# Kernel tuning notes

Measured on AMD Instinct MI355X. Metric: run time of the kernel, lower is better.

Reference implementation:

```python
import jax, jax.numpy as jnp
import numpy as np

B, L, V = 16, 2048, 64


def setup_inputs() -> dict:
    key = jax.random.key(0)
    k1, k2, k3, k4 = jax.random.split(key, 4)
    idx = jax.random.randint(k1, (B, L), 0, V)                      # tokens
    Wq_w = jax.random.normal(k2, (V, V), jnp.float32) * 0.02         # nn.Linear weight
    Wv_w = jax.random.normal(k3, (V, V), jnp.float32) * 0.02 + np.float32(np.e)  # Wv.weight (+e init)
    v_emb = jax.random.normal(k4, (L, 1), jnp.float32) * 0.02        # nn.Embedding(length, 1)
    return {"idx": idx, "Wq_w": Wq_w, "Wv_w": Wv_w, "v_emb": v_emb}


def reference(idx, Wq_w, Wv_w, v_emb):
    Lx = v_emb.shape[0]
    Vx = Wq_w.shape[0]
    # e = one_hot token embedding, [B, L, V]
    e = jax.nn.one_hot(idx, Vx, dtype=jnp.float32)
    i = jnp.arange(Lx)
    # pos[i, j] = max(i - j, 0); learned relative-position score table [L, L]
    pos = jnp.maximum(i[:, None] - i[None, :], 0)
    pos_embd = v_emb[pos, 0]
    causal = i[:, None] >= i[None, :]                                # tril mask
    # Attention block 1: scores are the learned position table (no QK^T)
    attn1 = jax.nn.softmax(jnp.where(causal, pos_embd, -jnp.inf), axis=-1)  # [L, L]
    l1 = jnp.einsum('ts,bsv->btv', attn1, e)                         # [B, L, V]
    # Attention block 2: Wq(e) @ l1^T, masked softmax, attn @ e * scalar
    q = jnp.einsum('btv,uv->btu', e, Wq_w)                           # F.linear: e @ Wq^T
    scores = jnp.einsum('btv,bsv->bts', q, l1)                       # [B, L, L]
    attn2 = jax.nn.softmax(jnp.where(causal, scores, -jnp.inf), axis=-1)
    l2 = jnp.einsum('bts,bsv->btv', attn2, e) * Wv_w[0, 0]           # logits [B, L, V]
    return l2
```

## Files before the change

### kernel.cpp

```cpp
#include <hip/hip_runtime.h>


#define LSEQ 2048
#define NB 16
#define NV 64
#define NC 32

typedef __attribute__((ext_vector_type(8))) short bf16x8;
typedef __attribute__((ext_vector_type(4))) float f32x4;

__device__ __forceinline__ unsigned short f2bf(float f) {
  unsigned int u = __float_as_uint(f);
  return (unsigned short)((u + 0x7FFFu + ((u >> 16) & 1u)) >> 16);
}

__global__ __launch_bounds__(256) void k_gather(const int* __restrict__ idx,
                                                const float* __restrict__ Wq,
                                                const float* __restrict__ v_emb,
                                                unsigned short* __restrict__ Agr,
                                                unsigned short* __restrict__ Ebf,
                                                float* __restrict__ S) {
  const int b = blockIdx.x >> 4;
  const int tile = blockIdx.x & 15;
  const int w = threadIdx.x >> 6;
  const int lane = threadIdx.x & 63;

  if (blockIdx.x == 0 && threadIdx.x < 64) {
    const int base = lane * 32;
    float e[32];
    float run = 0.f;
#pragma unroll
    for (int i = 0; i < 32; ++i) { e[i] = expf(v_emb[base + i]); run += e[i]; }
    float incl = run;
#pragma unroll
    for (int d = 1; d < 64; d <<= 1) {
      float up = __shfl_up(incl, d);
      if (lane >= d) incl += up;
    }
    float acc = incl - run;
#pragma unroll
    for (int i = 0; i < 32; ++i) {
      acc += e[i];
      Ebf[base + i] = f2bf(e[i]);
      S[base + i] = acc;
    }
  }

  const int k8base = tile * 16 + w * 4;
#pragma unroll
  for (int r = 0; r < 4; ++r) {
    const int k8 = k8base + r;
    unsigned short v[8];
#pragma unroll
    for (int j = 0; j < 8; ++j) {
      const int ii = idx[b * LSEQ + (2047 - (k8 * 8 + j))];
      v[j] = f2bf(Wq[ii * 64 + lane]);
    }
    uint4 st;
    st.x = (unsigned int)v[0] | ((unsigned int)v[1] << 16);
    st.y = (unsigned int)v[2] | ((unsigned int)v[3] << 16);
    st.z = (unsigned int)v[4] | ((unsigned int)v[5] << 16);
    st.w = (unsigned int)v[6] | ((unsigned int)v[7] << 16);
    *(uint4*)(Agr + ((size_t)(b * 256 + k8) * 64 + lane) * 8) = st;
  }
}

__global__ __launch_bounds__(256) void k_gemm(const unsigned short* __restrict__ Agr,
                                              const unsigned short* __restrict__ Ebf,
                                              const float* __restrict__ S,
                                              float* __restrict__ P) {
  __shared__ unsigned short GL0[2208];
  __shared__ unsigned short GL1[2176];
  __shared__ float red[16][64];
  __shared__ float red2[16][64];

  const int b  = blockIdx.y;
  const int bn = 63 - (int)blockIdx.x;
  const int n0 = bn * 32;
  const int tid = threadIdx.x;
  const int w = tid >> 6;
  const int lane = tid & 63;
  const int quad = lane >> 4;
  const int lm = lane & 15;
  const int nsub = w & 1;
  const int kh = w >> 1;

  {
    const int wend = n0 + 160;
    for (int i = 96 + tid; i < wend; i += 256) {
      const int e0 = i - 127;
      const int e1 = i - 126;
      GL0[i] = (e0 >= 0 && e0 < LSEQ) ? Ebf[e0] : (unsigned short)0;
      GL1[i] = (e1 >= 0 && e1 < LSEQ) ? Ebf[e1] : (unsigned short)0;
    }
  }
  __syncthreads();

  f32x4 acc[4];
#pragma unroll
  for (int mt = 0; mt < 4; ++mt) acc[mt] = (f32x4){0.f, 0.f, 0.f, 0.f};

  const int nbase = n0 + nsub * 16;
  const int sbase = nbase + lm - 1920;
  const int kstart = 2048 - (n0 + 32);
  const int iters = bn + 1;
  const unsigned short* __restrict__ abase = Agr + (size_t)b * 256 * 64 * 8;

  union AF { uint4 u; bf16x8 v; };
  union BF { unsigned int u[4]; bf16x8 v; };
  AF a[3][4];
  BF bb[3];

#define LOAD_FRAGS(J_, SL) do {                                             \
    const int k_ = kstart + (kh + 2 * (J_)) * 32;                           \
    const int kq8_ = (k_ >> 3) + quad;                                      \
    const unsigned short* ab_ = abase + ((size_t)kq8_ * 64 + lm) * 8;       \
    a[SL][0].u = *(const uint4*)(ab_ + 0 * 128);                            \
    a[SL][1].u = *(const uint4*)(ab_ + 1 * 128);                            \
    a[SL][2].u = *(const uint4*)(ab_ + 2 * 128);                            \
    a[SL][3].u = *(const uint4*)(ab_ + 3 * 128);                            \
    const int s_ = sbase + k_ + quad * 8;                                   \
    const unsigned int* gb_ = (s_ & 1) ? (const unsigned int*)GL1           \
                                       : (const unsigned int*)GL0;          \
    const int off_ = s_ >> 1;                                               \
    bb[SL].u[0] = gb_[off_ + 0]; bb[SL].u[1] = gb_[off_ + 1];               \
    bb[SL].u[2] = gb_[off_ + 2]; bb[SL].u[3] = gb_[off_ + 3];               \
  } while (0)

#define MFMA4(SL) do {                                                      \
    acc[0] = __builtin_amdgcn_mfma_f32_16x16x32_bf16(a[SL][0].v, bb[SL].v, acc[0], 0, 0, 0); \
    acc[1] = __builtin_amdgcn_mfma_f32_16x16x32_bf16(a[SL][1].v, bb[SL].v, acc[1], 0, 0, 0); \
    acc[2] = __builtin_amdgcn_mfma_f32_16x16x32_bf16(a[SL][2].v, bb[SL].v, acc[2], 0, 0, 0); \
    acc[3] = __builtin_amdgcn_mfma_f32_16x16x32_bf16(a[SL][3].v, bb[SL].v, acc[3], 0, 0, 0); \
  } while (0)

  const int J = (iters > kh) ? ((iters - kh + 1) >> 1) : 0;
  if (J > 0) {
    LOAD_FRAGS(0, 0);
    if (J > 1) LOAD_FRAGS(1, 1);
    int j = 0;
    while (true) {
      if (j + 2 < J) LOAD_FRAGS(j + 2, 2);
      MFMA4(0);
      if (++j >= J) break;
      if (j + 2 < J) LOAD_FRAGS(j + 2, 0);
      MFMA4(1);
      if (++j >= J) break;
      if (j + 2 < J) LOAD_FRAGS(j + 2, 1);
      MFMA4(2);
      if (++j >= J) break;
    }
  }
#undef LOAD_FRAGS
#undef MFMA4

  if (kh == 1) {
    float (*rd)[64] = nsub ? red2 : red;
#pragma unroll
    for (int mt = 0; mt < 4; ++mt)
#pragma unroll
      for (int r = 0; r < 4; ++r) rd[mt * 4 + r][lane] = acc[mt][r];
  }
  __syncthreads();
  if (kh == 0) {
    float (*rd)[64] = nsub ? red2 : red;
#pragma unroll
    for (int mt = 0; mt < 4; ++mt)
#pragma unroll
      for (int r = 0; r < 4; ++r) acc[mt][r] += rd[mt * 4 + r][lane];

    const float sinv = 1.0f / S[nbase + lm];
#pragma unroll
    for (int mt = 0; mt < 4; ++mt) {
#pragma unroll
      for (int r = 0; r < 4; ++r) {
        const int c = mt * 16 + quad * 4 + r;
        P[((size_t)(b * 64 + c)) * LSEQ + nbase + lm] = __expf(acc[mt][r] * sinv);
      }
    }
  }
}

__global__ __launch_bounds__(256) void k_scanemit(const int* __restrict__ idx,
                                                  const float* __restrict__ P,
                                                  const float* __restrict__ Wv,
                                                  float* __restrict__ out) {
  __shared__ float Hs[NC][65];
  __shared__ float bins[4][64];
  const int bc = blockIdx.x;
  const int b = bc >> 6;
  const int c = bc & 63;
  const int w = threadIdx.x >> 6;
  const int lane = threadIdx.x & 63;

  const float* __restrict__ prow = P + (size_t)bc * LSEQ;
  const int* __restrict__ irow = idx + b * LSEQ;

  float p[8]; int ii[8];
#pragma unroll
  for (int r = 0; r < 8; ++r) {
    const int ch = w * 8 + r;
    p[r] = prow[ch * 64 + lane];
    ii[r] = irow[ch * 64 + lane];
  }
  for (int i = threadIdx.x; i < NC * 65; i += 256) ((float*)Hs)[i] = 0.f;
  __syncthreads();
#pragma unroll
  for (int r = 0; r < 8; ++r) atomicAdd(&Hs[w * 8 + r][ii[r]], p[r]);
  __syncthreads();

  const int half = lane >> 5, l32 = lane & 31;
#pragma unroll
  for (int r = 0; r < 8; ++r) {
    const int v = w * 16 + r * 2 + half;
    const float h = Hs[l32][v];
    float x = h;
#pragma unroll
    for (int d = 1; d < 32; d <<= 1) {
      float up = __shfl_up(x, d, 32);
      if (l32 >= d) x += up;
    }
    Hs[l32][v] = x - h;
  }
  __syncthreads();

  const float wv = Wv[0];
#pragma unroll
  for (int r = 0; r < 8; ++r) {
    const int ch = w * 8 + r;
    unsigned long long m = __ballot(ii[r] == c);
    while (m) {
      const int srel = __builtin_ctzll(m);
      m &= m - 1;
      const int t = ch * 64 + srel;
      const float pm = (lane <= srel) ? p[r] : 0.f;
      bins[w][lane] = 0.f;
      __threadfence_block();
      atomicAdd(&bins[w][ii[r]], pm);
      __threadfence_block();
      const float bin = bins[w][lane] + Hs[ch][lane];
      float z = bin;
#pragma unroll
      for (int d = 1; d < 64; d <<= 1) z += __shfl_xor(z, d);
      out[((size_t)(b * LSEQ + t)) * 64 + lane] = wv * bin / z;
    }
  }
}

extern "C" void kernel_launch(void* const* d_in, const int* in_sizes, int n_in,
                              void* d_out, int out_size, void* d_ws, size_t ws_size,
                              hipStream_t stream) {
  const int* idx     = (const int*)d_in[0];
  const float* Wq    = (const float*)d_in[1];
  const float* Wv    = (const float*)d_in[2];
  const float* v_emb = (const float*)d_in[3];
  float* out = (float*)d_out;

  float* S = (float*)d_ws;
  float* P = S + LSEQ;
  unsigned short* Ebf = (unsigned short*)(P + (size_t)NB * NV * LSEQ);
  unsigned short* Agr = Ebf + LSEQ;

  k_gather<<<NB * 16, 256, 0, stream>>>(idx, Wq, v_emb, Agr, Ebf, S);
  k_gemm<<<dim3(64, NB), 256, 0, stream>>>(Agr, Ebf, S, P);
  k_scanemit<<<NB * NV, 256, 0, stream>>>(idx, P, Wv, out);
}
```

Measured before the change: 120.3 us.

## Halve GEMM N-tile and split M across waves to double block count

The GEMM kernel now uses 16-column N tiles instead of 32, launching 128x16 blocks. Each wave pair splits the 64 output channels in half (msub) rather than splitting N. Pipelining drops from triple to double buffering, and launch bounds request 8 blocks per CU. The aim is better load balance across CUs for the triangular causal workload and lower register pressure. The cost is more redundant A-fragment loads and a shallower prefetch.

```diff
diff --git a/kernel.cpp b/kernel.cpp
--- a/kernel.cpp
+++ b/kernel.cpp
@@ -65,28 +65,27 @@
   }
 }
 
-__global__ __launch_bounds__(256) void k_gemm(const unsigned short* __restrict__ Agr,
-                                              const unsigned short* __restrict__ Ebf,
-                                              const float* __restrict__ S,
-                                              float* __restrict__ P) {
+__global__ __launch_bounds__(256, 8) void k_gemm(const unsigned short* __restrict__ Agr,
+                                                 const unsigned short* __restrict__ Ebf,
+                                                 const float* __restrict__ S,
+                                                 float* __restrict__ P) {
   __shared__ unsigned short GL0[2208];
   __shared__ unsigned short GL1[2176];
-  __shared__ float red[16][64];
-  __shared__ float red2[16][64];
+  __shared__ float red[2][8][64];
 
   const int b  = blockIdx.y;
-  const int bn = 63 - (int)blockIdx.x;
-  const int n0 = bn * 32;
+  const int bn = 127 - (int)blockIdx.x;
+  const int n0 = bn * 16;
   const int tid = threadIdx.x;
   const int w = tid >> 6;
   const int lane = tid & 63;
   const int quad = lane >> 4;
   const int lm = lane & 15;
-  const int nsub = w & 1;
+  const int msub = w & 1;
   const int kh = w >> 1;
 
   {
-    const int wend = n0 + 160;
+    const int wend = n0 + 144;
     for (int i = 96 + tid; i < wend; i += 256) {
       const int e0 = i - 127;
       const int e1 = i - 126;
@@ -96,86 +95,72 @@
   }
   __syncthreads();
 
-  f32x4 acc[4];
-#pragma unroll
-  for (int mt = 0; mt < 4; ++mt) acc[mt] = (f32x4){0.f, 0.f, 0.f, 0.f};
-
-  const int nbase = n0 + nsub * 16;
-  const int sbase = nbase + lm - 1920;
-  const int kstart = 2048 - (n0 + 32);
-  const int iters = bn + 1;
+  f32x4 acc[2];
+  acc[0] = (f32x4){0.f, 0.f, 0.f, 0.f};
+  acc[1] = (f32x4){0.f, 0.f, 0.f, 0.f};
+
+  const int sbase = n0 + lm - 1920;
+  const int kext = (n0 + 16 + 31) & ~31;
+  const int kstart = 2048 - kext;
+  const int iters = kext >> 5;
   const unsigned short* __restrict__ abase = Agr + (size_t)b * 256 * 64 * 8;
+  const unsigned int* __restrict__ gb =
+      (sbase & 1) ? (const unsigned int*)GL1 : (const unsigned int*)GL0;
 
   union AF { uint4 u; bf16x8 v; };
   union BF { unsigned int u[4]; bf16x8 v; };
-  AF a[3][4];
-  BF bb[3];
+  AF a[2][2];
+  BF bb[2];
 
 #define LOAD_FRAGS(J_, SL) do {                                             \
     const int k_ = kstart + (kh + 2 * (J_)) * 32;                           \
     const int kq8_ = (k_ >> 3) + quad;                                      \
-    const unsigned short* ab_ = abase + ((size_t)kq8_ * 64 + lm) * 8;       \
+    const unsigned short* ab_ = abase + ((size_t)kq8_ * 64 + msub * 32 + lm) * 8; \
     a[SL][0].u = *(const uint4*)(ab_ + 0 * 128);                            \
     a[SL][1].u = *(const uint4*)(ab_ + 1 * 128);                            \
-    a[SL][2].u = *(const uint4*)(ab_ + 2 * 128);                            \
-    a[SL][3].u = *(const uint4*)(ab_ + 3 * 128);                            \
-    const int s_ = sbase + k_ + quad * 8;                                   \
-    const unsigned int* gb_ = (s_ & 1) ? (const unsigned int*)GL1           \
-                                       : (const unsigned int*)GL0;          \
-    const int off_ = s_ >> 1;                                               \
-    bb[SL].u[0] = gb_[off_ + 0]; bb[SL].u[1] = gb_[off_ + 1];               \
-    bb[SL].u[2] = gb_[off_ + 2]; bb[SL].u[3] = gb_[off_ + 3];               \
+    const int off_ = (sbase + k_ + quad * 8) >> 1;                          \
+    bb[SL].u[0] = gb[off_ + 0]; bb[SL].u[1] = gb[off_ + 1];                 \
+    bb[SL].u[2] = gb[off_ + 2]; bb[SL].u[3] = gb[off_ + 3];                 \
   } while (0)
 
-#define MFMA4(SL) do {                                                      \
+#define MFMA2(SL) do {                                                      \
     acc[0] = __builtin_amdgcn_mfma_f32_16x16x32_bf16(a[SL][0].v, bb[SL].v, acc[0], 0, 0, 0); \
     acc[1] = __builtin_amdgcn_mfma_f32_16x16x32_bf16(a[SL][1].v, bb[SL].v, acc[1], 0, 0, 0); \
-    acc[2] = __builtin_amdgcn_mfma_f32_16x16x32_bf16(a[SL][2].v, bb[SL].v, acc[2], 0, 0, 0); \
-    acc[3] = __builtin_amdgcn_mfma_f32_16x16x32_bf16(a[SL][3].v, bb[SL].v, acc[3], 0, 0, 0); \
   } while (0)
 
   const int J = (iters > kh) ? ((iters - kh + 1) >> 1) : 0;
   if (J > 0) {
     LOAD_FRAGS(0, 0);
-    if (J > 1) LOAD_FRAGS(1, 1);
     int j = 0;
     while (true) {
-      if (j + 2 < J) LOAD_FRAGS(j + 2, 2);
-      MFMA4(0);
+      if (j + 1 < J) LOAD_FRAGS(j + 1, (j + 1) & 1);
+      MFMA2(j & 1);
       if (++j >= J) break;
-      if (j + 2 < J) LOAD_FRAGS(j + 2, 0);
-      MFMA4(1);
-      if (++j >= J) break;
-      if (j + 2 < J) LOAD_FRAGS(j + 2, 1);
-      MFMA4(2);
-      if (++j >= J) break;
     }
   }
 #undef LOAD_FRAGS
-#undef MFMA4
+#undef MFMA2
 
   if (kh == 1) {
-    float (*rd)[64] = nsub ? red2 : red;
-#pragma unroll
-    for (int mt = 0; mt < 4; ++mt)
-#pragma unroll
-      for (int r = 0; r < 4; ++r) rd[mt * 4 + r][lane] = acc[mt][r];
+#pragma unroll
+    for (int mt = 0; mt < 2; ++mt)
+#pragma unroll
+      for (int r = 0; r < 4; ++r) red[msub][mt * 4 + r][lane] = acc[mt][r];
   }
   __syncthreads();
   if (kh == 0) {
-    float (*rd)[64] = nsub ? red2 : red;
-#pragma unroll
-    for (int mt = 0; mt < 4; ++mt)
-#pragma unroll
-      for (int r = 0; r < 4; ++r) acc[mt][r] += rd[mt * 4 + r][lane];
-
-    const float sinv = 1.0f / S[nbase + lm];
-#pragma unroll
-    for (int mt = 0; mt < 4; ++mt) {
+#pragma unroll
+    for (int mt = 0; mt < 2; ++mt)
+#pragma unroll
+      for (int r = 0; r < 4; ++r) acc[mt][r] += red[msub][mt * 4 + r][lane];
+
+    const float sinv = 1.0f / S[n0 + lm];
+#pragma unroll
+    for (int mt = 0; mt < 2; ++mt) {
 #pragma unroll
       for (int r = 0; r < 4; ++r) {
-        const int c = mt * 16 + quad * 4 + r;
-        P[((size_t)(b * 64 + c)) * LSEQ + nbase + lm] = __expf(acc[mt][r] * sinv);
+        const int c = msub * 32 + mt * 16 + quad * 4 + r;
+        P[((size_t)(b * 64 + c)) * LSEQ + n0 + lm] = __expf(acc[mt][r] * sinv);
       }
     }
   }
@@ -262,6 +247,6 @@
   unsigned short* Agr = Ebf + LSEQ;
 
   k_gather<<<NB * 16, 256, 0, stream>>>(idx, Wq, v_emb, Agr, Ebf, S);
-  k_gemm<<<dim3(64, NB), 256, 0, stream>>>(Agr, Ebf, S, P);
+  k_gemm<<<dim3(128, NB), 256, 0, stream>>>(Agr, Ebf, S, P);
   k_scanemit<<<NB * NV, 256, 0, stream>>>(idx, P, Wv, out);
 }
```

Result: slower. 298.0 us (+147.7%).
